# Kernel optimization log

Measured on AMD Instinct MI355X. Metric: run time of the kernel, lower is better.

## Reference

```python
import jax, jax.numpy as jnp
import numpy as np

# Config / sizes
N = 20000       # nodes
E = 320000      # edges (avg degree 16)
IN_DIM = 6      # node feature dim
PE = 8          # laplacian PE dims
ED = 4          # edge feature dim
H = 128         # hidden dim
OUT = 4         # output dim
L = 3           # message-passing layers
T = 3           # node types (typed encoders/decoders)


def mlp(z, W1, b1, W2, b2):
    # _make_mlp: Linear -> ReLU -> Linear
    return jax.nn.relu(z @ W1 + b1) @ W2 + b2


def typed_mlp(z, W1, b1, W2, b2, types):
    # W1: [T, Din, H]; compute all T branches, select per-node by type
    h = jax.nn.relu(jnp.einsum('ni,tih->tnh', z, W1) + b1[:, None, :])
    o = jnp.einsum('tnh,tho->tno', h, W2) + b2[:, None, :]
    onehot = jax.nn.one_hot(types, W1.shape[0], dtype=o.dtype)  # [N, T]
    return jnp.einsum('tno,nt->no', o, onehot)


def setup_inputs() -> dict:
    key = jax.random.key(0)
    ks = jax.random.split(key, 40)

    def w(k, shape, fan_in):
        return jax.random.normal(k, shape, dtype=jnp.float32) / np.float32(np.sqrt(fan_in))

    inp = {}
    inp['x'] = jax.random.normal(ks[0], (N, IN_DIM), dtype=jnp.float32)
    inp['pe'] = jax.random.normal(ks[1], (N, PE), dtype=jnp.float32)
    inp['edge_attr'] = jax.random.normal(ks[2], (E, ED), dtype=jnp.float32)
    # typed node encoders: (in_dim+pe_dims) -> H -> H
    inp['enc_W1'] = w(ks[3], (T, IN_DIM + PE, H), IN_DIM + PE)
    inp['enc_b1'] = jnp.zeros((T, H), jnp.float32)
    inp['enc_W2'] = w(ks[4], (T, H, H), H)
    inp['enc_b2'] = jnp.zeros((T, H), jnp.float32)
    # edge encoder: ED -> H -> H
    inp['ee_W1'] = w(ks[5], (ED, H), ED)
    inp['ee_b1'] = jnp.zeros((H,), jnp.float32)
    inp['ee_W2'] = w(ks[6], (H, H), H)
    inp['ee_b2'] = jnp.zeros((H,), jnp.float32)
    # per-layer edge update (3H->H->H), node update (2H->H->H), fusion (H->H->H)
    inp['eu_W1'] = w(ks[7], (L, 3 * H, H), 3 * H)
    inp['eu_b1'] = jnp.zeros((L, H), jnp.float32)
    inp['eu_W2'] = w(ks[8], (L, H, H), H)
    inp['eu_b2'] = jnp.zeros((L, H), jnp.float32)
    inp['nu_W1'] = w(ks[9], (L, 2 * H, H), 2 * H)
    inp['nu_b1'] = jnp.zeros((L, H), jnp.float32)
    inp['nu_W2'] = w(ks[10], (L, H, H), H)
    inp['nu_b2'] = jnp.zeros((L, H), jnp.float32)
    inp['fu_W1'] = w(ks[11], (L, H, H), H)
    inp['fu_b1'] = jnp.zeros((L, H), jnp.float32)
    inp['fu_W2'] = w(ks[12], (L, H, H), H)
    inp['fu_b2'] = jnp.zeros((L, H), jnp.float32)
    # typed decoders: H -> H -> OUT
    inp['dec_W1'] = w(ks[13], (T, H, H), H)
    inp['dec_b1'] = jnp.zeros((T, H), jnp.float32)
    inp['dec_W2'] = w(ks[14], (T, H, OUT), H)
    inp['dec_b2'] = jnp.zeros((T, OUT), jnp.float32)
    # int inputs
    inp['edge_index'] = jax.random.randint(ks[15], (2, E), 0, N)
    inp['node_types'] = jax.random.randint(ks[16], (N,), 0, T)
    return inp


def reference(x, pe, edge_attr,
              enc_W1, enc_b1, enc_W2, enc_b2,
              ee_W1, ee_b1, ee_W2, ee_b2,
              eu_W1, eu_b1, eu_W2, eu_b2,
              nu_W1, nu_b1, nu_W2, nu_b2,
              fu_W1, fu_b1, fu_W2, fu_b2,
              dec_W1, dec_b1, dec_W2, dec_b2,
              edge_index, node_types):
    n = x.shape[0]
    src, dst = edge_index[0], edge_index[1]
    # typed node encode on [x || pe]
    h_nodes = typed_mlp(jnp.concatenate([x, pe], axis=-1),
                        enc_W1, enc_b1, enc_W2, enc_b2, node_types)
    # edge encode
    h_edges = mlp(edge_attr, ee_W1, ee_b1, ee_W2, ee_b2)
    num_layers = eu_W1.shape[0]
    for l in range(num_layers):
        # gather endpoint states, edge MLP, residual on edges
        m_edge = mlp(jnp.concatenate([h_nodes[src], h_nodes[dst], h_edges], axis=-1),
                     eu_W1[l], eu_b1[l], eu_W2[l], eu_b2[l])
        h_edges = h_edges + m_edge
        # scatter-add aggregation to destination nodes (index_add_)
        m_node = jax.ops.segment_sum(h_edges, dst, num_segments=n)
        # node update + residual, then fusion (dropout is eval/identity)
        upd = mlp(jnp.concatenate([h_nodes, m_node], axis=-1),
                  nu_W1[l], nu_b1[l], nu_W2[l], nu_b2[l])
        local = h_nodes + upd
        h_nodes = mlp(local, fu_W1[l], fu_b1[l], fu_W2[l], fu_b2[l])
    # typed decode
    out = typed_mlp(h_nodes, dec_W1, dec_b1, dec_W2, dec_b2, node_types)
    return out
```

## Files before the change

kernel.cpp:

```cpp
#include <hip/hip_runtime.h>
#include <hip/hip_bf16.h>

typedef __hip_bfloat16 bf16;
typedef __attribute__((ext_vector_type(8))) short short8;
typedef __attribute__((ext_vector_type(4))) float floatx4;

#define HDIM 128
#define NCANON 27

__device__ __forceinline__ float b2f(bf16 v) { return __bfloat162float(v); }
__device__ __forceinline__ float s2f(short s) {
  return __uint_as_float(((unsigned int)(unsigned short)s) << 16);
}

__global__ void detect_kernel(const unsigned short* __restrict__ xraw, int* __restrict__ flag) {
  int j = threadIdx.x;
  unsigned short u = xraw[2 * j];
  int e = (u >> 7) & 0xFF;
  int ok = (u == 0) || (e >= 100 && e <= 140);
  unsigned long long m = __ballot(ok);
  if (j == 0) flag[0] = (__popcll(m) >= 48) ? 1 : 0;
}

struct CanonDesc {
  const void* src[NCANON];
  int prefix[NCANON + 1];
};

__global__ void canon_kernel(CanonDesc d, const int* __restrict__ flag,
                             bf16* __restrict__ out, int total) {
  int t = blockIdx.x * 256 + threadIdx.x;
  if (t >= total) return;
  int ti = 0;
  while (d.prefix[ti + 1] <= t) ti++;
  int off = t - d.prefix[ti];
  if (flag[0]) out[t] = ((const bf16*)d.src[ti])[off];
  else         out[t] = __float2bfloat16(((const float*)d.src[ti])[off]);
}

__global__ void emit_kernel(const bf16* __restrict__ canon_out, const int* __restrict__ flag,
                            void* __restrict__ d_out, int n) {
  int t = blockIdx.x * 256 + threadIdx.x;
  if (t >= n) return;
  if (flag[0]) ((bf16*)d_out)[t] = canon_out[t];
  else         ((float*)d_out)[t] = __bfloat162float(canon_out[t]);
}

__global__ void hist_kernel(const int* __restrict__ dst, int* __restrict__ cnt, int E) {
  int e = blockIdx.x * 256 + threadIdx.x;
  if (e < E) atomicAdd(&cnt[dst[e]], 1);
}

__global__ void scan1_kernel(const int* __restrict__ cnt, int* __restrict__ bsum, int n) {
  int tid = threadIdx.x, lane = tid & 63, wave = tid >> 6;
  int i = blockIdx.x * 256 + tid;
  int v = (i < n) ? cnt[i] : 0;
  #pragma unroll
  for (int d = 32; d; d >>= 1) v += __shfl_down(v, d);
  __shared__ int ws[4];
  if (lane == 0) ws[wave] = v;
  __syncthreads();
  if (tid == 0) bsum[blockIdx.x] = ws[0] + ws[1] + ws[2] + ws[3];
}

__global__ void scan2_kernel(int* __restrict__ bsum, int nb) {
  int lane = threadIdx.x;
  int a0 = (lane < nb) ? bsum[lane] : 0;
  int b0 = (64 + lane < nb) ? bsum[64 + lane] : 0;
  int a = a0, b = b0;
  #pragma unroll
  for (int d = 1; d < 64; d <<= 1) { int t = __shfl_up(a, d); if (lane >= d) a += t; }
  int totA = __shfl(a, 63);
  #pragma unroll
  for (int d = 1; d < 64; d <<= 1) { int t = __shfl_up(b, d); if (lane >= d) b += t; }
  int totB = __shfl(b, 63);
  if (lane < nb) bsum[lane] = a - a0;
  if (64 + lane < nb) bsum[64 + lane] = b - b0 + totA;
  if (lane == 0) bsum[nb] = totA + totB;
}

__global__ void scan3_kernel(const int* __restrict__ cnt, const int* __restrict__ bsum,
                             int* __restrict__ row_start, int n, int nb) {
  __shared__ int sh[256];
  int tid = threadIdx.x;
  int i = blockIdx.x * 256 + tid;
  int v = (i < n) ? cnt[i] : 0;
  sh[tid] = v;
  __syncthreads();
  #pragma unroll
  for (int off = 1; off < 256; off <<= 1) {
    int t = (tid >= off) ? sh[tid - off] : 0;
    __syncthreads();
    sh[tid] += t;
    __syncthreads();
  }
  if (i < n) row_start[i] = bsum[blockIdx.x] + sh[tid] - v;
  if (blockIdx.x == 0 && tid == 0) row_start[n] = bsum[nb];
}

__global__ void scatter_kernel(const int* __restrict__ src, const int* __restrict__ dst,
                               const int* __restrict__ row_start, int* __restrict__ cursor,
                               int* __restrict__ sortedE, int* __restrict__ srcS,
                               int* __restrict__ dstS, int E) {
  int e = blockIdx.x * 256 + threadIdx.x;
  if (e < E) {
    int d = dst[e];
    int pos = row_start[d] + atomicAdd(&cursor[d], 1);
    sortedE[pos] = e;
    srcS[pos] = src[e];
    dstS[pos] = d;
  }
}

__global__ void tcount_kernel(const int* __restrict__ types, int* __restrict__ bcnt, int n) {
  int i = blockIdx.x * 256 + threadIdx.x;
  int lane = threadIdx.x & 63, wave = threadIdx.x >> 6;
  int t = (i < n) ? types[i] : -1;
  __shared__ int wc[4][3];
  unsigned long long m0 = __ballot(t == 0);
  unsigned long long m1 = __ballot(t == 1);
  unsigned long long m2 = __ballot(t == 2);
  if (lane == 0) {
    wc[wave][0] = __popcll(m0); wc[wave][1] = __popcll(m1); wc[wave][2] = __popcll(m2);
  }
  __syncthreads();
  if (threadIdx.x < 3)
    bcnt[blockIdx.x * 3 + threadIdx.x] =
        wc[0][threadIdx.x] + wc[1][threadIdx.x] + wc[2][threadIdx.x] + wc[3][threadIdx.x];
}

__global__ void tscan_kernel(const int* __restrict__ bcnt, int* __restrict__ boff,
                             int* __restrict__ ts, int nb, int n) {
  int lane = threadIdx.x;
  __shared__ int tots[3];
  for (int t = 0; t < 3; t++) {
    int a0 = (lane < nb) ? bcnt[lane * 3 + t] : 0;
    int b0 = (64 + lane < nb) ? bcnt[(64 + lane) * 3 + t] : 0;
    int a = a0, b = b0;
    #pragma unroll
    for (int d = 1; d < 64; d <<= 1) { int x = __shfl_up(a, d); if (lane >= d) a += x; }
    int totA = __shfl(a, 63);
    #pragma unroll
    for (int d = 1; d < 64; d <<= 1) { int x = __shfl_up(b, d); if (lane >= d) b += x; }
    int totB = __shfl(b, 63);
    if (lane < nb) boff[lane * 3 + t] = a - a0;
    if (64 + lane < nb) boff[(64 + lane) * 3 + t] = b - b0 + totA;
    if (lane == 0) tots[t] = totA + totB;
  }
  __syncthreads();
  int tot0 = tots[0], tot1 = tots[1];
  if (lane == 0) { ts[0] = 0; ts[1] = tot0; ts[2] = tot0 + tot1; ts[3] = n; }
  for (int idx = lane; idx < nb; idx += 64) {
    boff[idx * 3 + 1] += tot0;
    boff[idx * 3 + 2] += tot0 + tot1;
  }
}

__global__ void tscatter2_kernel(const int* __restrict__ types, const int* __restrict__ boff,
                                 int* __restrict__ perm, int n) {
  int i = blockIdx.x * 256 + threadIdx.x;
  int lane = threadIdx.x & 63, wave = threadIdx.x >> 6;
  int t = (i < n) ? types[i] : -1;
  __shared__ int wc[4][3];
  unsigned long long m0 = __ballot(t == 0);
  unsigned long long m1 = __ballot(t == 1);
  unsigned long long m2 = __ballot(t == 2);
  if (lane == 0) {
    wc[wave][0] = __popcll(m0); wc[wave][1] = __popcll(m1); wc[wave][2] = __popcll(m2);
  }
  __syncthreads();
  if (i >= n) return;
  unsigned long long mt = (t == 0) ? m0 : ((t == 1) ? m1 : m2);
  unsigned long long below = (lane == 0) ? 0ull : ((1ull << lane) - 1ull);
  int laneRank = __popcll(mt & below);
  int waveOff = 0;
  for (int w = 0; w < wave; w++) waveOff += wc[w][t];
  perm[boff[blockIdx.x * 3 + t] + waveOff + laneRank] = i;
}

__global__ void aggregate_kernel(const bf16* __restrict__ h_edges, const int* __restrict__ row_start,
                                 bf16* __restrict__ m_node, int n) {
  int node = blockIdx.x * 4 + (threadIdx.x >> 6);
  if (node >= n) return;
  int lane = threadIdx.x & 63;
  int chunk = lane & 15;
  int sub = lane >> 4;
  int s = row_start[node], e = row_start[node + 1];
  float acc[8];
  #pragma unroll
  for (int j = 0; j < 8; j++) acc[j] = 0.f;
  for (int p = s + sub; p < e; p += 4) {
    short8 v = *(const short8*)(h_edges + (size_t)p * HDIM + chunk * 8);
    #pragma unroll
    for (int j = 0; j < 8; j++) acc[j] += s2f(v[j]);
  }
  #pragma unroll
  for (int j = 0; j < 8; j++) {
    acc[j] += __shfl_xor(acc[j], 16);
    acc[j] += __shfl_xor(acc[j], 32);
  }
  if (sub == 0) {
    short8 o;
    #pragma unroll
    for (int j = 0; j < 8; j++) o[j] = (short)__bfloat16_as_ushort(__float2bfloat16(acc[j]));
    *(short8*)(m_node + (size_t)node * HDIM + chunk * 8) = o;
  }
}

struct PackJob { const bf16* src; bf16* dst; int Ksrc; int KS; int srcCols; };
struct PackJobs { PackJob j[40]; };

__global__ void pack_all_kernel(PackJobs J) {
  PackJob job = J.j[blockIdx.y];
  int idx = blockIdx.x * 256 + threadIdx.x;
  int total = 8 * job.KS * 64;
  if (idx >= total) return;
  int lane = idx & 63;
  int ks = (idx >> 6) % job.KS;
  int ct = idx / (64 * job.KS);
  bf16* o = job.dst + (size_t)idx * 8;
  int ncol = ct * 16 + (lane & 15);
  int kb = ks * 32 + ((lane >> 4) & 3) * 8;
  #pragma unroll
  for (int jj = 0; jj < 8; jj++) {
    int k = kb + jj;
    o[jj] = (k < job.Ksrc && ncol < job.srcCols)
              ? job.src[(size_t)k * job.srcCols + ncol] : __float2bfloat16(0.f);
  }
}

__global__ void __launch_bounds__(256) ygemm_kernel(
    const bf16* __restrict__ X,
    const bf16* __restrict__ WpA, const bf16* __restrict__ WpB,
    bf16* __restrict__ outA, bf16* __restrict__ outB, int M) {
  const bf16* Wp = blockIdx.y ? WpB : WpA;
  bf16* outp = blockIdx.y ? outB : outA;
  constexpr int BM = 64, RT = 4, SK = 136;
  __shared__ bf16 Zt[BM * SK];
  const int tid = threadIdx.x;
  const int lane = tid & 63, wave = tid >> 6, colq = lane & 15, quad = lane >> 4;
  const int row0 = blockIdx.x * BM;
  {
    int row = tid >> 2, sub = tid & 3;
    int gr = row0 + row;
    bool ok = gr < M;
    #pragma unroll
    for (int j = 0; j < 4; j++) {
      int seg = j * 4 + sub;
      uint4 v = {0u, 0u, 0u, 0u};
      if (ok) v = *(const uint4*)(X + (size_t)gr * HDIM + seg * 8);
      *(uint4*)(&Zt[row * SK + seg * 8]) = v;
    }
  }
  __syncthreads();
  floatx4 acc[RT][2];
  #pragma unroll
  for (int rt = 0; rt < RT; rt++)
    #pragma unroll
    for (int c = 0; c < 2; c++) acc[rt][c] = (floatx4){0.f, 0.f, 0.f, 0.f};
  #pragma unroll
  for (int ks = 0; ks < 4; ks++) {
    short8 bfr0 = *(const short8*)(Wp + (((size_t)(wave * 2 + 0) * 4 + ks) * 64 + lane) * 8);
    short8 bfr1 = *(const short8*)(Wp + (((size_t)(wave * 2 + 1) * 4 + ks) * 64 + lane) * 8);
    #pragma unroll
    for (int rt = 0; rt < RT; rt++) {
      short8 a = *(const short8*)(&Zt[(rt * 16 + colq) * SK + ks * 32 + quad * 8]);
      acc[rt][0] = __builtin_amdgcn_mfma_f32_16x16x32_bf16(a, bfr0, acc[rt][0], 0, 0, 0);
      acc[rt][1] = __builtin_amdgcn_mfma_f32_16x16x32_bf16(a, bfr1, acc[rt][1], 0, 0, 0);
    }
  }
  #pragma unroll
  for (int c = 0; c < 2; c++) {
    int col = wave * 32 + c * 16 + colq;
    #pragma unroll
    for (int rt = 0; rt < RT; rt++)
      #pragma unroll
      for (int r = 0; r < 4; r++) {
        int grow = row0 + rt * 16 + quad * 4 + r;
        if (grow < M) outp[(size_t)grow * HDIM + col] = __float2bfloat16(acc[rt][c][r]);
      }
  }
}

template<int BM>
__global__ void __launch_bounds__(256) eu_kernel(
    const bf16* __restrict__ he, const bf16* __restrict__ ysrc, const bf16* __restrict__ ydst,
    const int* __restrict__ srcS, const int* __restrict__ dstS,
    const bf16* __restrict__ W1p, const bf16* __restrict__ b1v,
    const bf16* __restrict__ W2p, const bf16* __restrict__ b2v,
    bf16* __restrict__ outp, int M) {
  constexpr int RT = BM / 16;
  constexpr int SK = 264;
  __shared__ bf16 Zt[BM * SK];
  const int tid = threadIdx.x;
  const int lane = tid & 63, wave = tid >> 6, colq = lane & 15, quad = lane >> 4;
  const int row0 = blockIdx.x * BM;
  constexpr int TPR = 256 / BM;
  {
    int row = tid / TPR, sub = tid % TPR;
    int gr = row0 + row;
    bool ok = gr < M;
    int g0 = ok ? srcS[gr] : 0;
    int g1 = ok ? dstS[gr] : 0;
    #pragma unroll
    for (int j = 0; j < 32 / TPR; j++) {
      int c = j * TPR + sub;
      int part = c >> 4, seg = c & 15;
      if (part == 0) {
        short8 o = {0, 0, 0, 0, 0, 0, 0, 0};
        if (ok) {
          short8 a = *(const short8*)(ysrc + (size_t)g0 * HDIM + seg * 8);
          short8 b = *(const short8*)(ydst + (size_t)g1 * HDIM + seg * 8);
          #pragma unroll
          for (int k = 0; k < 8; k++)
            o[k] = (short)__bfloat16_as_ushort(__float2bfloat16(s2f(a[k]) + s2f(b[k])));
        }
        *(short8*)(&Zt[row * SK + seg * 8]) = o;
      } else {
        uint4 v = {0u, 0u, 0u, 0u};
        if (ok) v = *(const uint4*)(he + (size_t)gr * HDIM + seg * 8);
        *(uint4*)(&Zt[row * SK + 128 + seg * 8]) = v;
      }
    }
  }
  __syncthreads();

  floatx4 acc[RT][2];
  #pragma unroll
  for (int rt = 0; rt < RT; rt++)
    #pragma unroll
    for (int c = 0; c < 2; c++) acc[rt][c] = (floatx4){0.f, 0.f, 0.f, 0.f};
  #pragma unroll
  for (int ks = 0; ks < 4; ks++) {
    short8 bfr0 = *(const short8*)(W1p + (((size_t)(wave * 2 + 0) * 4 + ks) * 64 + lane) * 8);
    short8 bfr1 = *(const short8*)(W1p + (((size_t)(wave * 2 + 1) * 4 + ks) * 64 + lane) * 8);
    #pragma unroll
    for (int rt = 0; rt < RT; rt++) {
      short8 a = *(const short8*)(&Zt[(rt * 16 + colq) * SK + 128 + ks * 32 + quad * 8]);
      acc[rt][0] = __builtin_amdgcn_mfma_f32_16x16x32_bf16(a, bfr0, acc[rt][0], 0, 0, 0);
      acc[rt][1] = __builtin_amdgcn_mfma_f32_16x16x32_bf16(a, bfr1, acc[rt][1], 0, 0, 0);
    }
  }
  #pragma unroll
  for (int c = 0; c < 2; c++) {
    int col = wave * 32 + c * 16 + colq;
    float bv = b2f(b1v[col]);
    #pragma unroll
    for (int rt = 0; rt < RT; rt++)
      #pragma unroll
      for (int r = 0; r < 4; r++) {
        int lrow = rt * 16 + quad * 4 + r;
        float v = acc[rt][c][r] + bv + b2f(Zt[lrow * SK + col]);
        Zt[lrow * SK + col] = __float2bfloat16(fmaxf(v, 0.f));
      }
  }
  __syncthreads();

  floatx4 acc2[RT][2];
  #pragma unroll
  for (int rt = 0; rt < RT; rt++)
    #pragma unroll
    for (int c = 0; c < 2; c++) acc2[rt][c] = (floatx4){0.f, 0.f, 0.f, 0.f};
  #pragma unroll
  for (int ks = 0; ks < 4; ks++) {
    short8 bfr0 = *(const short8*)(W2p + (((size_t)(wave * 2 + 0) * 4 + ks) * 64 + lane) * 8);
    short8 bfr1 = *(const short8*)(W2p + (((size_t)(wave * 2 + 1) * 4 + ks) * 64 + lane) * 8);
    #pragma unroll
    for (int rt = 0; rt < RT; rt++) {
      short8 a = *(const short8*)(&Zt[(rt * 16 + colq) * SK + ks * 32 + quad * 8]);
      acc2[rt][0] = __builtin_amdgcn_mfma_f32_16x16x32_bf16(a, bfr0, acc2[rt][0], 0, 0, 0);
      acc2[rt][1] = __builtin_amdgcn_mfma_f32_16x16x32_bf16(a, bfr1, acc2[rt][1], 0, 0, 0);
    }
  }
  #pragma unroll
  for (int c = 0; c < 2; c++) {
    int col = wave * 32 + c * 16 + colq;
    float bv = b2f(b2v[col]);
    #pragma unroll
    for (int rt = 0; rt < RT; rt++)
      #pragma unroll
      for (int r = 0; r < 4; r++) {
        int lrow = rt * 16 + quad * 4 + r;
        int grow = row0 + lrow;
        if (grow < M) {
          float v = acc2[rt][c][r] + bv + b2f(Zt[lrow * SK + 128 + col]);
          outp[(size_t)grow * HDIM + col] = __float2bfloat16(v);
        }
      }
  }
}

template<int KS1, bool DEC>
__global__ void __launch_bounds__(256) typed_kernel(
    const bf16* __restrict__ in0, const bf16* __restrict__ in1,
    const int* __restrict__ perm, const int* __restrict__ ts,
    const bf16* __restrict__ W1p, int w1s, const bf16* __restrict__ b1v, int b1s,
    const bf16* __restrict__ W2p, int w2s, const bf16* __restrict__ b2v, int b2s,
    bf16* __restrict__ outp) {
  constexpr int BM = 64, RT = 4;
  constexpr int SK = KS1 * 32 + 8;
  constexpr int HS = 136;
  int t = blockIdx.y;
  int rs = ts[t], re = ts[t + 1];
  int row0 = rs + blockIdx.x * BM;
  if (row0 >= re) return;
  __shared__ bf16 Zt[BM * SK];
  __shared__ bf16 Hid[BM * HS];
  __shared__ int gIdx[BM];
  const int tid = threadIdx.x;
  const int lane = tid & 63, wave = tid >> 6, colq = lane & 15, quad = lane >> 4;
  for (int i = tid; i < BM; i += 256) gIdx[i] = (row0 + i < re) ? perm[row0 + i] : -1;
  __syncthreads();
  if (DEC) {
    int row = tid >> 2, sub = tid & 3;
    int g = gIdx[row];
    #pragma unroll
    for (int j = 0; j < 4; j++) {
      int seg = j * 4 + sub;
      uint4 v = {0u, 0u, 0u, 0u};
      if (g >= 0) v = *(const uint4*)(in0 + (size_t)g * HDIM + seg * 8);
      *(uint4*)(&Zt[row * SK + seg * 8]) = v;
    }
  } else {
    for (int i = tid; i < BM * 32; i += 256) {
      int row = i >> 5, k = i & 31;
      int g = gIdx[row];
      bf16 v = __float2bfloat16(0.f);
      if (g >= 0 && k < 14) v = (k < 6) ? in0[(size_t)g * 6 + k] : in1[(size_t)g * 8 + (k - 6)];
      Zt[row * SK + k] = v;
    }
  }
  __syncthreads();

  const bf16* W1t = W1p + (size_t)t * w1s;
  const bf16* W2t = W2p + (size_t)t * w2s;
  floatx4 acc[RT][2];
  #pragma unroll
  for (int rt = 0; rt < RT; rt++)
    #pragma unroll
    for (int c = 0; c < 2; c++) acc[rt][c] = (floatx4){0.f, 0.f, 0.f, 0.f};
  #pragma unroll
  for (int ks = 0; ks < KS1; ks++) {
    short8 bfr0 = *(const short8*)(W1t + (((size_t)(wave * 2 + 0) * KS1 + ks) * 64 + lane) * 8);
    short8 bfr1 = *(const short8*)(W1t + (((size_t)(wave * 2 + 1) * KS1 + ks) * 64 + lane) * 8);
    #pragma unroll
    for (int rt = 0; rt < RT; rt++) {
      short8 a = *(const short8*)(&Zt[(rt * 16 + colq) * SK + ks * 32 + quad * 8]);
      acc[rt][0] = __builtin_amdgcn_mfma_f32_16x16x32_bf16(a, bfr0, acc[rt][0], 0, 0, 0);
      acc[rt][1] = __builtin_amdgcn_mfma_f32_16x16x32_bf16(a, bfr1, acc[rt][1], 0, 0, 0);
    }
  }
  #pragma unroll
  for (int c = 0; c < 2; c++) {
    int col = wave * 32 + c * 16 + colq;
    float bv = b2f(b1v[t * b1s + col]);
    #pragma unroll
    for (int rt = 0; rt < RT; rt++)
      #pragma unroll
      for (int r = 0; r < 4; r++) {
        float v = acc[rt][c][r] + bv;
        Hid[(rt * 16 + quad * 4 + r) * HS + col] = __float2bfloat16(fmaxf(v, 0.f));
      }
  }
  __syncthreads();

  floatx4 acc2[RT][2];
  #pragma unroll
  for (int rt = 0; rt < RT; rt++)
    #pragma unroll
    for (int c = 0; c < 2; c++) acc2[rt][c] = (floatx4){0.f, 0.f, 0.f, 0.f};
  #pragma unroll
  for (int ks = 0; ks < 4; ks++) {
    short8 bfr0 = *(const short8*)(W2t + (((size_t)(wave * 2 + 0) * 4 + ks) * 64 + lane) * 8);
    short8 bfr1 = *(const short8*)(W2t + (((size_t)(wave * 2 + 1) * 4 + ks) * 64 + lane) * 8);
    #pragma unroll
    for (int rt = 0; rt < RT; rt++) {
      short8 a = *(const short8*)(&Hid[(rt * 16 + colq) * HS + ks * 32 + quad * 8]);
      acc2[rt][0] = __builtin_amdgcn_mfma_f32_16x16x32_bf16(a, bfr0, acc2[rt][0], 0, 0, 0);
      acc2[rt][1] = __builtin_amdgcn_mfma_f32_16x16x32_bf16(a, bfr1, acc2[rt][1], 0, 0, 0);
    }
  }
  if (DEC) {
    if (wave == 0 && colq < 4) {
      float bv = b2f(b2v[t * b2s + colq]);
      #pragma unroll
      for (int rt = 0; rt < RT; rt++)
        #pragma unroll
        for (int r = 0; r < 4; r++) {
          int g = gIdx[rt * 16 + quad * 4 + r];
          if (g >= 0) outp[(size_t)g * 4 + colq] = __float2bfloat16(acc2[rt][0][r] + bv);
        }
    }
  } else {
    #pragma unroll
    for (int c = 0; c < 2; c++) {
      int col = wave * 32 + c * 16 + colq;
      float bv = b2f(b2v[t * b2s + col]);
      #pragma unroll
      for (int rt = 0; rt < RT; rt++)
        #pragma unroll
        for (int r = 0; r < 4; r++) {
          int g = gIdx[rt * 16 + quad * 4 + r];
          if (g >= 0) outp[(size_t)g * HDIM + col] = __float2bfloat16(acc2[rt][c][r] + bv);
        }
    }
  }
}

template<int NPARTS, int KS1, int RES_PART, int BM, int HID_OFF, bool ATTR4>
__global__ void __launch_bounds__(256) mlp2_kernel(
    const bf16* __restrict__ p0, const int* __restrict__ idx0,
    const bf16* __restrict__ p1,
    const bf16* __restrict__ W1p, const bf16* __restrict__ b1v,
    const bf16* __restrict__ W2p, const bf16* __restrict__ b2v,
    bf16* __restrict__ outp, int M) {
  constexpr int RT = BM / 16;
  constexpr int SK = NPARTS * 128 + 8;
  __shared__ bf16 Zt[BM * SK];
  bf16* Hid = &Zt[HID_OFF];
  const int tid = threadIdx.x;
  const int lane = tid & 63, wave = tid >> 6, colq = lane & 15, quad = lane >> 4;
  const int row0 = blockIdx.x * BM;

  if (ATTR4) {
    for (int i = tid; i < BM * 4; i += 256) {
      int row = i >> 2, seg = i & 3;
      int gr = row0 + row;
      uint4 val = {0u, 0u, 0u, 0u};
      if (seg == 0 && gr < M) {
        int g = idx0 ? idx0[gr] : gr;
        uint2 v = *(const uint2*)(p0 + (size_t)g * 4);
        val.x = v.x; val.y = v.y;
      }
      *(uint4*)(&Zt[row * SK + seg * 8]) = val;
    }
  } else {
    constexpr int TPR = 256 / BM;
    constexpr int PT = NPARTS * 16 / TPR;
    int row = tid / TPR, sub = tid % TPR;
    int gr = row0 + row;
    bool ok = (gr < M);
    #pragma unroll
    for (int j = 0; j < PT; j++) {
      int c = j * TPR + sub;
      int part = c >> 4, seg = c & 15;
      uint4 val = {0u, 0u, 0u, 0u};
      if (ok) {
        const bf16* p = (part == 0) ? p0 : p1;
        val = *(const uint4*)(p + (size_t)gr * HDIM + seg * 8);
      }
      *(uint4*)(&Zt[row * SK + part * 128 + seg * 8]) = val;
    }
  }
  __syncthreads();

  floatx4 acc[RT][2];
  #pragma unroll
  for (int rt = 0; rt < RT; rt++)
    #pragma unroll
    for (int c = 0; c < 2; c++) acc[rt][c] = (floatx4){0.f, 0.f, 0.f, 0.f};
  #pragma unroll
  for (int ks = 0; ks < KS1; ks++) {
    short8 bfr0 = *(const short8*)(W1p + (((size_t)(wave * 2 + 0) * KS1 + ks) * 64 + lane) * 8);
    short8 bfr1 = *(const short8*)(W1p + (((size_t)(wave * 2 + 1) * KS1 + ks) * 64 + lane) * 8);
    #pragma unroll
    for (int rt = 0; rt < RT; rt++) {
      short8 a = *(const short8*)(&Zt[(rt * 16 + colq) * SK + ks * 32 + quad * 8]);
      acc[rt][0] = __builtin_amdgcn_mfma_f32_16x16x32_bf16(a, bfr0, acc[rt][0], 0, 0, 0);
      acc[rt][1] = __builtin_amdgcn_mfma_f32_16x16x32_bf16(a, bfr1, acc[rt][1], 0, 0, 0);
    }
  }
  __syncthreads();

  #pragma unroll
  for (int c = 0; c < 2; c++) {
    int col = wave * 32 + c * 16 + colq;
    float bv = b2f(b1v[col]);
    #pragma unroll
    for (int rt = 0; rt < RT; rt++)
      #pragma unroll
      for (int r = 0; r < 4; r++) {
        float v = acc[rt][c][r] + bv;
        Hid[(rt * 16 + quad * 4 + r) * SK + col] = __float2bfloat16(fmaxf(v, 0.f));
      }
  }
  __syncthreads();

  floatx4 acc2[RT][2];
  #pragma unroll
  for (int rt = 0; rt < RT; rt++)
    #pragma unroll
    for (int c = 0; c < 2; c++) acc2[rt][c] = (floatx4){0.f, 0.f, 0.f, 0.f};
  #pragma unroll
  for (int ks = 0; ks < 4; ks++) {
    short8 bfr0 = *(const short8*)(W2p + (((size_t)(wave * 2 + 0) * 4 + ks) * 64 + lane) * 8);
    short8 bfr1 = *(const short8*)(W2p + (((size_t)(wave * 2 + 1) * 4 + ks) * 64 + lane) * 8);
    #pragma unroll
    for (int rt = 0; rt < RT; rt++) {
      short8 a = *(const short8*)(&Hid[(rt * 16 + colq) * SK + ks * 32 + quad * 8]);
      acc2[rt][0] = __builtin_amdgcn_mfma_f32_16x16x32_bf16(a, bfr0, acc2[rt][0], 0, 0, 0);
      acc2[rt][1] = __builtin_amdgcn_mfma_f32_16x16x32_bf16(a, bfr1, acc2[rt][1], 0, 0, 0);
    }
  }
  #pragma unroll
  for (int c = 0; c < 2; c++) {
    int col = wave * 32 + c * 16 + colq;
    float bv = b2f(b2v[col]);
    #pragma unroll
    for (int rt = 0; rt < RT; rt++)
      #pragma unroll
      for (int r = 0; r < 4; r++) {
        int lrow = rt * 16 + quad * 4 + r;
        int grow = row0 + lrow;
        if (grow < M) {
          float v = acc2[rt][c][r] + bv;
          if constexpr (RES_PART >= 0)
            v += b2f(Zt[lrow * SK + RES_PART * 128 + col]);
          outp[(size_t)grow * HDIM + col] = __float2bfloat16(v);
        }
      }
  }
}

extern "C" void kernel_launch(void* const* d_in, const int* in_sizes, int n_in,
                              void* d_out, int out_size, void* d_ws, size_t ws_size,
                              hipStream_t stream) {
  const int* edge_index = (const int*)d_in[27];
  const int* node_types = (const int*)d_in[28];
  const int N = in_sizes[28];
  const int E = in_sizes[2] / 4;
  const int L = in_sizes[12] / HDIM;
  const int* srcI = edge_index;
  const int* dstI = edge_index + E;

  CanonDesc cd;
  int total = 0;
  for (int i = 0; i < NCANON; i++) { cd.src[i] = d_in[i]; cd.prefix[i] = total; total += in_sizes[i]; }
  cd.prefix[NCANON] = total;

  char* wsb = (char*)d_ws;
  size_t off = 0;
  auto alloc = [&](size_t bytes) -> void* {
    void* p = wsb + off;
    off += (bytes + 255) & ~(size_t)255;
    return p;
  };
  int*  flag      = (int*)alloc(256);
  bf16* arena     = (bf16*)alloc((size_t)total * 2);
  bf16* h_nodes   = (bf16*)alloc((size_t)N * HDIM * 2);
  bf16* h_edges   = (bf16*)alloc((size_t)E * HDIM * 2);
  bf16* m_node    = (bf16*)alloc((size_t)N * HDIM * 2);
  bf16* localb    = (bf16*)alloc((size_t)N * HDIM * 2);
  bf16* ysrcb     = (bf16*)alloc((size_t)N * HDIM * 2);
  bf16* ydstb     = (bf16*)alloc((size_t)N * HDIM * 2);
  bf16* canon_out = (bf16*)alloc((size_t)out_size * 2);
  int* counts     = (int*)alloc((size_t)N * 4);
  int* cursor     = (int*)alloc((size_t)N * 4);
  int* row_start  = (int*)alloc((size_t)(N + 1) * 4);
  int* bsum       = (int*)alloc(260 * 4);
  int* sortedE    = (int*)alloc((size_t)E * 4);
  int* srcS       = (int*)alloc((size_t)E * 4);
  int* dstS       = (int*)alloc((size_t)E * 4);
  int* bcntT      = (int*)alloc(512 * 4);
  int* boffT      = (int*)alloc(512 * 4);
  int* tsArr      = (int*)alloc(64);
  int* permT      = (int*)alloc((size_t)N * 4);
  bf16* eeW1p  = (bf16*)alloc(4096 * 2);
  bf16* eeW2p  = (bf16*)alloc(16384 * 2);
  bf16* encW1p = (bf16*)alloc(3 * 4096 * 2);
  bf16* encW2p = (bf16*)alloc(3 * 16384 * 2);
  bf16* decW1p = (bf16*)alloc(3 * 16384 * 2);
  bf16* decW2p = (bf16*)alloc(3 * 16384 * 2);
  bf16* euW1a  = (bf16*)alloc((size_t)L * 16384 * 2);
  bf16* euW1b  = (bf16*)alloc((size_t)L * 16384 * 2);
  bf16* euW1c  = (bf16*)alloc((size_t)L * 16384 * 2);
  bf16* euW2p  = (bf16*)alloc((size_t)L * 16384 * 2);
  bf16* nuW1p  = (bf16*)alloc((size_t)L * 32768 * 2);
  bf16* nuW2p  = (bf16*)alloc((size_t)L * 16384 * 2);
  bf16* fuW1p  = (bf16*)alloc((size_t)L * 16384 * 2);
  bf16* fuW2p  = (bf16*)alloc((size_t)L * 16384 * 2);

  const bf16* cX     = arena + cd.prefix[0];
  const bf16* cPE    = arena + cd.prefix[1];
  const bf16* cEA    = arena + cd.prefix[2];
  const bf16* cEncW1 = arena + cd.prefix[3];
  const bf16* cEncB1 = arena + cd.prefix[4];
  const bf16* cEncW2 = arena + cd.prefix[5];
  const bf16* cEncB2 = arena + cd.prefix[6];
  const bf16* cEeW1  = arena + cd.prefix[7];
  const bf16* cEeB1  = arena + cd.prefix[8];
  const bf16* cEeW2  = arena + cd.prefix[9];
  const bf16* cEeB2  = arena + cd.prefix[10];
  const bf16* cEuW1  = arena + cd.prefix[11];
  const bf16* cEuB1  = arena + cd.prefix[12];
  const bf16* cEuW2  = arena + cd.prefix[13];
  const bf16* cEuB2  = arena + cd.prefix[14];
  const bf16* cNuW1  = arena + cd.prefix[15];
  const bf16* cNuB1  = arena + cd.prefix[16];
  const bf16* cNuW2  = arena + cd.prefix[17];
  const bf16* cNuB2  = arena + cd.prefix[18];
  const bf16* cFuW1  = arena + cd.prefix[19];
  const bf16* cFuB1  = arena + cd.prefix[20];
  const bf16* cFuW2  = arena + cd.prefix[21];
  const bf16* cFuB2  = arena + cd.prefix[22];
  const bf16* cDecW1 = arena + cd.prefix[23];
  const bf16* cDecB1 = arena + cd.prefix[24];
  const bf16* cDecW2 = arena + cd.prefix[25];
  const bf16* cDecB2 = arena + cd.prefix[26];

  detect_kernel<<<1, 64, 0, stream>>>((const unsigned short*)d_in[0], flag);
  canon_kernel<<<(total + 255) / 256, 256, 0, stream>>>(cd, flag, arena, total);

  hipMemsetAsync(counts, 0, (size_t)N * 4, stream);
  hipMemsetAsync(cursor, 0, (size_t)N * 4, stream);

  PackJobs PJ;
  int nj = 0;
  PJ.j[nj++] = {cEeW1, eeW1p, 4, 1, 128};
  PJ.j[nj++] = {cEeW2, eeW2p, 128, 4, 128};
  for (int l = 0; l < L; l++) {
    const bf16* w1 = cEuW1 + (size_t)l * 384 * HDIM;
    PJ.j[nj++] = {w1,                 euW1a + (size_t)l * 16384, 128, 4, 128};
    PJ.j[nj++] = {w1 + 128 * HDIM,    euW1b + (size_t)l * 16384, 128, 4, 128};
    PJ.j[nj++] = {w1 + 256 * HDIM,    euW1c + (size_t)l * 16384, 128, 4, 128};
    PJ.j[nj++] = {cEuW2 + (size_t)l * HDIM * HDIM, euW2p + (size_t)l * 16384, 128, 4, 128};
    PJ.j[nj++] = {cNuW1 + (size_t)l * 256 * HDIM,  nuW1p + (size_t)l * 32768, 256, 8, 128};
    PJ.j[nj++] = {cNuW2 + (size_t)l * HDIM * HDIM, nuW2p + (size_t)l * 16384, 128, 4, 128};
    PJ.j[nj++] = {cFuW1 + (size_t)l * HDIM * HDIM, fuW1p + (size_t)l * 16384, 128, 4, 128};
    PJ.j[nj++] = {cFuW2 + (size_t)l * HDIM * HDIM, fuW2p + (size_t)l * 16384, 128, 4, 128};
  }
  for (int t = 0; t < 3; t++) {
    PJ.j[nj++] = {cEncW1 + (size_t)t * 14 * HDIM,   encW1p + (size_t)t * 4096, 14, 1, 128};
    PJ.j[nj++] = {cEncW2 + (size_t)t * HDIM * HDIM, encW2p + (size_t)t * 16384, 128, 4, 128};
    PJ.j[nj++] = {cDecW1 + (size_t)t * HDIM * HDIM, decW1p + (size_t)t * 16384, 128, 4, 128};
    PJ.j[nj++] = {cDecW2 + (size_t)t * HDIM * 4,    decW2p + (size_t)t * 16384, 128, 4, 4};
  }
  pack_all_kernel<<<dim3(16, nj), 256, 0, stream>>>(PJ);

  int nb = (N + 255) / 256;
  hist_kernel<<<(E + 255) / 256, 256, 0, stream>>>(dstI, counts, E);
  scan1_kernel<<<nb, 256, 0, stream>>>(counts, bsum, N);
  scan2_kernel<<<1, 64, 0, stream>>>(bsum, nb);
  scan3_kernel<<<nb, 256, 0, stream>>>(counts, bsum, row_start, N, nb);
  scatter_kernel<<<(E + 255) / 256, 256, 0, stream>>>(srcI, dstI, row_start, cursor,
                                                      sortedE, srcS, dstS, E);
  tcount_kernel<<<nb, 256, 0, stream>>>(node_types, bcntT, N);
  tscan_kernel<<<1, 64, 0, stream>>>(bcntT, boffT, tsArr, nb, N);
  tscatter2_kernel<<<nb, 256, 0, stream>>>(node_types, boffT, permT, N);

  int ngrid64 = (N + 63) / 64;
  typed_kernel<1, false><<<dim3(ngrid64, 3), 256, 0, stream>>>(
      cX, cPE, permT, tsArr, encW1p, 4096, cEncB1, HDIM,
      encW2p, 16384, cEncB2, HDIM, h_nodes);

  int egrid32  = (E + 31) / 32;
  int egrid128 = (E + 127) / 128;
  int ngrid128 = (N + 127) / 128;

  mlp2_kernel<1, 1, -1, 128, 0, true><<<egrid128, 256, 0, stream>>>(
      cEA, sortedE, nullptr, eeW1p, cEeB1, eeW2p, cEeB2, h_edges, E);

  for (int l = 0; l < L; l++) {
    ygemm_kernel<<<dim3(ngrid64, 2), 256, 0, stream>>>(
        h_nodes, euW1a + (size_t)l * 16384, euW1b + (size_t)l * 16384, ysrcb, ydstb, N);
    eu_kernel<32><<<egrid32, 256, 0, stream>>>(
        h_edges, ysrcb, ydstb, srcS, dstS,
        euW1c + (size_t)l * 16384, cEuB1 + l * HDIM,
        euW2p + (size_t)l * 16384, cEuB2 + l * HDIM, h_edges, E);
    aggregate_kernel<<<(N + 3) / 4, 256, 0, stream>>>(h_edges, row_start, m_node, N);
    mlp2_kernel<2, 8, 0, 64, 128, false><<<ngrid64, 256, 0, stream>>>(
        h_nodes, nullptr, m_node,
        nuW1p + (size_t)l * 32768, cNuB1 + l * HDIM,
        nuW2p + (size_t)l * 16384, cNuB2 + l * HDIM, localb, N);
    mlp2_kernel<1, 4, -1, 128, 0, false><<<ngrid128, 256, 0, stream>>>(
        localb, nullptr, nullptr,
        fuW1p + (size_t)l * 16384, cFuB1 + l * HDIM,
        fuW2p + (size_t)l * 16384, cFuB2 + l * HDIM, h_nodes, N);
  }

  typed_kernel<4, true><<<dim3(ngrid64, 3), 256, 0, stream>>>(
      h_nodes, nullptr, permT, tsArr, decW1p, 16384, cDecB1, HDIM,
      decW2p, 16384, cDecB2, 4, canon_out);
  emit_kernel<<<(out_size + 255) / 256, 256, 0, stream>>>(canon_out, flag, d_out, out_size);
  (void)n_in; (void)ws_size;
}
```

Baseline: 537.5 us.

## Fuse edge aggregation into edge update and merge node/fusion MLPs

```diff
diff --git a/kernel.cpp b/kernel.cpp
--- a/kernel.cpp
+++ b/kernel.cpp
@@ -11,6 +11,9 @@
 __device__ __forceinline__ float b2f(bf16 v) { return __bfloat162float(v); }
 __device__ __forceinline__ float s2f(short s) {
   return __uint_as_float(((unsigned int)(unsigned short)s) << 16);
+}
+__device__ __forceinline__ short f2s(float f) {
+  return (short)__bfloat16_as_ushort(__float2bfloat16(f));
 }
 
 __global__ void detect_kernel(const unsigned short* __restrict__ xraw, int* __restrict__ flag) {
@@ -176,35 +179,6 @@
   int waveOff = 0;
   for (int w = 0; w < wave; w++) waveOff += wc[w][t];
   perm[boff[blockIdx.x * 3 + t] + waveOff + laneRank] = i;
-}
-
-__global__ void aggregate_kernel(const bf16* __restrict__ h_edges, const int* __restrict__ row_start,
-                                 bf16* __restrict__ m_node, int n) {
-  int node = blockIdx.x * 4 + (threadIdx.x >> 6);
-  if (node >= n) return;
-  int lane = threadIdx.x & 63;
-  int chunk = lane & 15;
-  int sub = lane >> 4;
-  int s = row_start[node], e = row_start[node + 1];
-  float acc[8];
-  #pragma unroll
-  for (int j = 0; j < 8; j++) acc[j] = 0.f;
-  for (int p = s + sub; p < e; p += 4) {
-    short8 v = *(const short8*)(h_edges + (size_t)p * HDIM + chunk * 8);
-    #pragma unroll
-    for (int j = 0; j < 8; j++) acc[j] += s2f(v[j]);
-  }
-  #pragma unroll
-  for (int j = 0; j < 8; j++) {
-    acc[j] += __shfl_xor(acc[j], 16);
-    acc[j] += __shfl_xor(acc[j], 32);
-  }
-  if (sub == 0) {
-    short8 o;
-    #pragma unroll
-    for (int j = 0; j < 8; j++) o[j] = (short)__bfloat16_as_ushort(__float2bfloat16(acc[j]));
-    *(short8*)(m_node + (size_t)node * HDIM + chunk * 8) = o;
-  }
 }
 
 struct PackJob { const bf16* src; bf16* dst; int Ksrc; int KS; int srcCols; };
@@ -288,10 +262,11 @@
     const int* __restrict__ srcS, const int* __restrict__ dstS,
     const bf16* __restrict__ W1p, const bf16* __restrict__ b1v,
     const bf16* __restrict__ W2p, const bf16* __restrict__ b2v,
-    bf16* __restrict__ outp, int M) {
+    bf16* __restrict__ outp, float* __restrict__ mnode, int M) {
   constexpr int RT = BM / 16;
   constexpr int SK = 264;
   __shared__ bf16 Zt[BM * SK];
+  __shared__ int dstLds[BM];
   const int tid = threadIdx.x;
   const int lane = tid & 63, wave = tid >> 6, colq = lane & 15, quad = lane >> 4;
   const int row0 = blockIdx.x * BM;
@@ -302,6 +277,7 @@
     bool ok = gr < M;
     int g0 = ok ? srcS[gr] : 0;
     int g1 = ok ? dstS[gr] : 0;
+    if (sub == 0) dstLds[row] = ok ? g1 : -1;
     #pragma unroll
     for (int j = 0; j < 32 / TPR; j++) {
       int c = j * TPR + sub;
@@ -312,8 +288,7 @@
           short8 a = *(const short8*)(ysrc + (size_t)g0 * HDIM + seg * 8);
           short8 b = *(const short8*)(ydst + (size_t)g1 * HDIM + seg * 8);
           #pragma unroll
-          for (int k = 0; k < 8; k++)
-            o[k] = (short)__bfloat16_as_ushort(__float2bfloat16(s2f(a[k]) + s2f(b[k])));
+          for (int k = 0; k < 8; k++) o[k] = f2s(s2f(a[k]) + s2f(b[k]));
         }
         *(short8*)(&Zt[row * SK + seg * 8]) = o;
       } else {
@@ -382,10 +357,184 @@
       for (int r = 0; r < 4; r++) {
         int lrow = rt * 16 + quad * 4 + r;
         int grow = row0 + lrow;
-        if (grow < M) {
-          float v = acc2[rt][c][r] + bv + b2f(Zt[lrow * SK + 128 + col]);
-          outp[(size_t)grow * HDIM + col] = __float2bfloat16(v);
+        float v = acc2[rt][c][r] + bv + b2f(Zt[lrow * SK + 128 + col]);
+        bf16 vb = __float2bfloat16(v);
+        Zt[lrow * SK + 128 + col] = vb;
+        if (grow < M) outp[(size_t)grow * HDIM + col] = vb;
+      }
+  }
+  __syncthreads();
+
+  if (tid < 128) {
+    int col = tid;
+    float s = 0.f;
+    int runDst = dstLds[0];
+    bool touchStart = true;
+    for (int r = 0; r < BM; r++) {
+      int d = dstLds[r];
+      if (d != runDst) {
+        if (runDst >= 0) {
+          float* mp = &mnode[(size_t)runDst * HDIM + col];
+          if (touchStart) atomicAdd(mp, s); else *mp = s;
         }
+        runDst = d; s = 0.f; touchStart = false;
+      }
+      s += b2f(Zt[r * SK + 128 + col]);
+    }
+    if (runDst >= 0) atomicAdd(&mnode[(size_t)runDst * HDIM + col], s);
+  }
+}
+
+__global__ void __launch_bounds__(256) node_kernel(
+    const bf16* __restrict__ h_nodes, const float* __restrict__ mnode,
+    const bf16* __restrict__ nuW1, const bf16* __restrict__ nuB1,
+    const bf16* __restrict__ nuW2, const bf16* __restrict__ nuB2,
+    const bf16* __restrict__ fuW1, const bf16* __restrict__ fuB1,
+    const bf16* __restrict__ fuW2, const bf16* __restrict__ fuB2,
+    bf16* __restrict__ outp, int M) {
+  constexpr int BM = 64, RT = 4, SK = 264;
+  __shared__ bf16 Zt[BM * SK];
+  const int tid = threadIdx.x;
+  const int lane = tid & 63, wave = tid >> 6, colq = lane & 15, quad = lane >> 4;
+  const int row0 = blockIdx.x * BM;
+  {
+    int row = tid >> 2, sub = tid & 3;
+    int gr = row0 + row;
+    bool ok = gr < M;
+    #pragma unroll
+    for (int j = 0; j < 8; j++) {
+      int c = j * 4 + sub;
+      int part = c >> 4, seg = c & 15;
+      if (part == 0) {
+        uint4 v = {0u, 0u, 0u, 0u};
+        if (ok) v = *(const uint4*)(h_nodes + (size_t)gr * HDIM + seg * 8);
+        *(uint4*)(&Zt[row * SK + seg * 8]) = v;
+      } else {
+        short8 o = {0, 0, 0, 0, 0, 0, 0, 0};
+        if (ok) {
+          const float* mp = mnode + (size_t)gr * HDIM + seg * 8;
+          #pragma unroll
+          for (int k = 0; k < 8; k++) o[k] = f2s(mp[k]);
+        }
+        *(short8*)(&Zt[row * SK + 128 + seg * 8]) = o;
+      }
+    }
+  }
+  __syncthreads();
+
+  floatx4 acc[RT][2];
+  #pragma unroll
+  for (int rt = 0; rt < RT; rt++)
+    #pragma unroll
+    for (int c = 0; c < 2; c++) acc[rt][c] = (floatx4){0.f, 0.f, 0.f, 0.f};
+  #pragma unroll
+  for (int ks = 0; ks < 8; ks++) {
+    short8 bfr0 = *(const short8*)(nuW1 + (((size_t)(wave * 2 + 0) * 8 + ks) * 64 + lane) * 8);
+    short8 bfr1 = *(const short8*)(nuW1 + (((size_t)(wave * 2 + 1) * 8 + ks) * 64 + lane) * 8);
+    #pragma unroll
+    for (int rt = 0; rt < RT; rt++) {
+      short8 a = *(const short8*)(&Zt[(rt * 16 + colq) * SK + ks * 32 + quad * 8]);
+      acc[rt][0] = __builtin_amdgcn_mfma_f32_16x16x32_bf16(a, bfr0, acc[rt][0], 0, 0, 0);
+      acc[rt][1] = __builtin_amdgcn_mfma_f32_16x16x32_bf16(a, bfr1, acc[rt][1], 0, 0, 0);
+    }
+  }
+  __syncthreads();
+  #pragma unroll
+  for (int c = 0; c < 2; c++) {
+    int col = wave * 32 + c * 16 + colq;
+    float bv = b2f(nuB1[col]);
+    #pragma unroll
+    for (int rt = 0; rt < RT; rt++)
+      #pragma unroll
+      for (int r = 0; r < 4; r++)
+        Zt[(rt * 16 + quad * 4 + r) * SK + 128 + col] =
+            __float2bfloat16(fmaxf(acc[rt][c][r] + bv, 0.f));
+  }
+  __syncthreads();
+
+  #pragma unroll
+  for (int rt = 0; rt < RT; rt++)
+    #pragma unroll
+    for (int c = 0; c < 2; c++) acc[rt][c] = (floatx4){0.f, 0.f, 0.f, 0.f};
+  #pragma unroll
+  for (int ks = 0; ks < 4; ks++) {
+    short8 bfr0 = *(const short8*)(nuW2 + (((size_t)(wave * 2 + 0) * 4 + ks) * 64 + lane) * 8);
+    short8 bfr1 = *(const short8*)(nuW2 + (((size_t)(wave * 2 + 1) * 4 + ks) * 64 + lane) * 8);
+    #pragma unroll
+    for (int rt = 0; rt < RT; rt++) {
+      short8 a = *(const short8*)(&Zt[(rt * 16 + colq) * SK + 128 + ks * 32 + quad * 8]);
+      acc[rt][0] = __builtin_amdgcn_mfma_f32_16x16x32_bf16(a, bfr0, acc[rt][0], 0, 0, 0);
+      acc[rt][1] = __builtin_amdgcn_mfma_f32_16x16x32_bf16(a, bfr1, acc[rt][1], 0, 0, 0);
+    }
+  }
+  #pragma unroll
+  for (int c = 0; c < 2; c++) {
+    int col = wave * 32 + c * 16 + colq;
+    float bv = b2f(nuB2[col]);
+    #pragma unroll
+    for (int rt = 0; rt < RT; rt++)
+      #pragma unroll
+      for (int r = 0; r < 4; r++) {
+        int lrow = rt * 16 + quad * 4 + r;
+        float v = acc[rt][c][r] + bv + b2f(Zt[lrow * SK + col]);
+        Zt[lrow * SK + col] = __float2bfloat16(v);
+      }
+  }
+  __syncthreads();
+
+  #pragma unroll
+  for (int rt = 0; rt < RT; rt++)
+    #pragma unroll
+    for (int c = 0; c < 2; c++) acc[rt][c] = (floatx4){0.f, 0.f, 0.f, 0.f};
+  #pragma unroll
+  for (int ks = 0; ks < 4; ks++) {
+    short8 bfr0 = *(const short8*)(fuW1 + (((size_t)(wave * 2 + 0) * 4 + ks) * 64 + lane) * 8);
+    short8 bfr1 = *(const short8*)(fuW1 + (((size_t)(wave * 2 + 1) * 4 + ks) * 64 + lane) * 8);
+    #pragma unroll
+    for (int rt = 0; rt < RT; rt++) {
+      short8 a = *(const short8*)(&Zt[(rt * 16 + colq) * SK + ks * 32 + quad * 8]);
+      acc[rt][0] = __builtin_amdgcn_mfma_f32_16x16x32_bf16(a, bfr0, acc[rt][0], 0, 0, 0);
+      acc[rt][1] = __builtin_amdgcn_mfma_f32_16x16x32_bf16(a, bfr1, acc[rt][1], 0, 0, 0);
+    }
+  }
+  #pragma unroll
+  for (int c = 0; c < 2; c++) {
+    int col = wave * 32 + c * 16 + colq;
+    float bv = b2f(fuB1[col]);
+    #pragma unroll
+    for (int rt = 0; rt < RT; rt++)
+      #pragma unroll
+      for (int r = 0; r < 4; r++)
+        Zt[(rt * 16 + quad * 4 + r) * SK + 128 + col] =
+            __float2bfloat16(fmaxf(acc[rt][c][r] + bv, 0.f));
+  }
+  __syncthreads();
+
+  #pragma unroll
+  for (int rt = 0; rt < RT; rt++)
+    #pragma unroll
+    for (int c = 0; c < 2; c++) acc[rt][c] = (floatx4){0.f, 0.f, 0.f, 0.f};
+  #pragma unroll
+  for (int ks = 0; ks < 4; ks++) {
+    short8 bfr0 = *(const short8*)(fuW2 + (((size_t)(wave * 2 + 0) * 4 + ks) * 64 + lane) * 8);
+    short8 bfr1 = *(const short8*)(fuW2 + (((size_t)(wave * 2 + 1) * 4 + ks) * 64 + lane) * 8);
+    #pragma unroll
+    for (int rt = 0; rt < RT; rt++) {
+      short8 a = *(const short8*)(&Zt[(rt * 16 + colq) * SK + 128 + ks * 32 + quad * 8]);
+      acc[rt][0] = __builtin_amdgcn_mfma_f32_16x16x32_bf16(a, bfr0, acc[rt][0], 0, 0, 0);
+      acc[rt][1] = __builtin_amdgcn_mfma_f32_16x16x32_bf16(a, bfr1, acc[rt][1], 0, 0, 0);
+    }
+  }
+  #pragma unroll
+  for (int c = 0; c < 2; c++) {
+    int col = wave * 32 + c * 16 + colq;
+    float bv = b2f(fuB2[col]);
+    #pragma unroll
+    for (int rt = 0; rt < RT; rt++)
+      #pragma unroll
+      for (int r = 0; r < 4; r++) {
+        int grow = row0 + rt * 16 + quad * 4 + r;
+        if (grow < M) outp[(size_t)grow * HDIM + col] = __float2bfloat16(acc[rt][c][r] + bv);
       }
   }
 }
@@ -507,50 +656,29 @@
   }
 }
 
-template<int NPARTS, int KS1, int RES_PART, int BM, int HID_OFF, bool ATTR4>
-__global__ void __launch_bounds__(256) mlp2_kernel(
+template<int BM>
+__global__ void __launch_bounds__(256) ee_kernel(
     const bf16* __restrict__ p0, const int* __restrict__ idx0,
-    const bf16* __restrict__ p1,
     const bf16* __restrict__ W1p, const bf16* __restrict__ b1v,
     const bf16* __restrict__ W2p, const bf16* __restrict__ b2v,
     bf16* __restrict__ outp, int M) {
   constexpr int RT = BM / 16;
-  constexpr int SK = NPARTS * 128 + 8;
+  constexpr int SK = 136;
   __shared__ bf16 Zt[BM * SK];
-  bf16* Hid = &Zt[HID_OFF];
   const int tid = threadIdx.x;
   const int lane = tid & 63, wave = tid >> 6, colq = lane & 15, quad = lane >> 4;
   const int row0 = blockIdx.x * BM;
 
-  if (ATTR4) {
-    for (int i = tid; i < BM * 4; i += 256) {
-      int row = i >> 2, seg = i & 3;
-      int gr = row0 + row;
-      uint4 val = {0u, 0u, 0u, 0u};
-      if (seg == 0 && gr < M) {
-        int g = idx0 ? idx0[gr] : gr;
-        uint2 v = *(const uint2*)(p0 + (size_t)g * 4);
-        val.x = v.x; val.y = v.y;
-      }
-      *(uint4*)(&Zt[row * SK + seg * 8]) = val;
-    }
-  } else {
-    constexpr int TPR = 256 / BM;
-    constexpr int PT = NPARTS * 16 / TPR;
-    int row = tid / TPR, sub = tid % TPR;
+  for (int i = tid; i < BM * 4; i += 256) {
+    int row = i >> 2, seg = i & 3;
     int gr = row0 + row;
-    bool ok = (gr < M);
-    #pragma unroll
-    for (int j = 0; j < PT; j++) {
-      int c = j * TPR + sub;
-      int part = c >> 4, seg = c & 15;
-      uint4 val = {0u, 0u, 0u, 0u};
-      if (ok) {
-        const bf16* p = (part == 0) ? p0 : p1;
-        val = *(const uint4*)(p + (size_t)gr * HDIM + seg * 8);
-      }
-      *(uint4*)(&Zt[row * SK + part * 128 + seg * 8]) = val;
-    }
+    uint4 val = {0u, 0u, 0u, 0u};
+    if (seg == 0 && gr < M) {
+      int g = idx0 ? idx0[gr] : gr;
+      uint2 v = *(const uint2*)(p0 + (size_t)g * 4);
+      val.x = v.x; val.y = v.y;
+    }
+    *(uint4*)(&Zt[row * SK + seg * 8]) = val;
   }
   __syncthreads();
 
@@ -559,19 +687,17 @@
   for (int rt = 0; rt < RT; rt++)
     #pragma unroll
     for (int c = 0; c < 2; c++) acc[rt][c] = (floatx4){0.f, 0.f, 0.f, 0.f};
-  #pragma unroll
-  for (int ks = 0; ks < KS1; ks++) {
-    short8 bfr0 = *(const short8*)(W1p + (((size_t)(wave * 2 + 0) * KS1 + ks) * 64 + lane) * 8);
-    short8 bfr1 = *(const short8*)(W1p + (((size_t)(wave * 2 + 1) * KS1 + ks) * 64 + lane) * 8);
-    #pragma unroll
-    for (int rt = 0; rt < RT; rt++) {
-      short8 a = *(const short8*)(&Zt[(rt * 16 + colq) * SK + ks * 32 + quad * 8]);
+  {
+    short8 bfr0 = *(const short8*)(W1p + (((size_t)(wave * 2 + 0)) * 64 + lane) * 8);
+    short8 bfr1 = *(const short8*)(W1p + (((size_t)(wave * 2 + 1)) * 64 + lane) * 8);
+    #pragma unroll
+    for (int rt = 0; rt < RT; rt++) {
+      short8 a = *(const short8*)(&Zt[(rt * 16 + colq) * SK + quad * 8]);
       acc[rt][0] = __builtin_amdgcn_mfma_f32_16x16x32_bf16(a, bfr0, acc[rt][0], 0, 0, 0);
       acc[rt][1] = __builtin_amdgcn_mfma_f32_16x16x32_bf16(a, bfr1, acc[rt][1], 0, 0, 0);
     }
   }
   __syncthreads();
-
   #pragma unroll
   for (int c = 0; c < 2; c++) {
     int col = wave * 32 + c * 16 + colq;
@@ -579,10 +705,9 @@
     #pragma unroll
     for (int rt = 0; rt < RT; rt++)
       #pragma unroll
-      for (int r = 0; r < 4; r++) {
-        float v = acc[rt][c][r] + bv;
-        Hid[(rt * 16 + quad * 4 + r) * SK + col] = __float2bfloat16(fmaxf(v, 0.f));
-      }
+      for (int r = 0; r < 4; r++)
+        Zt[(rt * 16 + quad * 4 + r) * SK + col] =
+            __float2bfloat16(fmaxf(acc[rt][c][r] + bv, 0.f));
   }
   __syncthreads();
 
@@ -597,7 +722,7 @@
     short8 bfr1 = *(const short8*)(W2p + (((size_t)(wave * 2 + 1) * 4 + ks) * 64 + lane) * 8);
     #pragma unroll
     for (int rt = 0; rt < RT; rt++) {
-      short8 a = *(const short8*)(&Hid[(rt * 16 + colq) * SK + ks * 32 + quad * 8]);
+      short8 a = *(const short8*)(&Zt[(rt * 16 + colq) * SK + ks * 32 + quad * 8]);
       acc2[rt][0] = __builtin_amdgcn_mfma_f32_16x16x32_bf16(a, bfr0, acc2[rt][0], 0, 0, 0);
       acc2[rt][1] = __builtin_amdgcn_mfma_f32_16x16x32_bf16(a, bfr1, acc2[rt][1], 0, 0, 0);
     }
@@ -610,14 +735,9 @@
     for (int rt = 0; rt < RT; rt++)
       #pragma unroll
       for (int r = 0; r < 4; r++) {
-        int lrow = rt * 16 + quad * 4 + r;
-        int grow = row0 + lrow;
-        if (grow < M) {
-          float v = acc2[rt][c][r] + bv;
-          if constexpr (RES_PART >= 0)
-            v += b2f(Zt[lrow * SK + RES_PART * 128 + col]);
-          outp[(size_t)grow * HDIM + col] = __float2bfloat16(v);
-        }
+        int grow = row0 + rt * 16 + quad * 4 + r;
+        if (grow < M)
+          outp[(size_t)grow * HDIM + col] = __float2bfloat16(acc2[rt][c][r] + bv);
       }
   }
 }
@@ -649,8 +769,7 @@
   bf16* arena     = (bf16*)alloc((size_t)total * 2);
   bf16* h_nodes   = (bf16*)alloc((size_t)N * HDIM * 2);
   bf16* h_edges   = (bf16*)alloc((size_t)E * HDIM * 2);
-  bf16* m_node    = (bf16*)alloc((size_t)N * HDIM * 2);
-  bf16* localb    = (bf16*)alloc((size_t)N * HDIM * 2);
+  float* m_node   = (float*)alloc((size_t)N * HDIM * 4);
   bf16* ysrcb     = (bf16*)alloc((size_t)N * HDIM * 2);
   bf16* ydstb     = (bf16*)alloc((size_t)N * HDIM * 2);
   bf16* canon_out = (bf16*)alloc((size_t)out_size * 2);
@@ -755,25 +874,22 @@
 
   int egrid32  = (E + 31) / 32;
   int egrid128 = (E + 127) / 128;
-  int ngrid128 = (N + 127) / 128;
-
-  mlp2_kernel<1, 1, -1, 128, 0, true><<<egrid128, 256, 0, stream>>>(
-      cEA, sortedE, nullptr, eeW1p, cEeB1, eeW2p, cEeB2, h_edges, E);
+
+  ee_kernel<128><<<egrid128, 256, 0, stream>>>(
+      cEA, sortedE, eeW1p, cEeB1, eeW2p, cEeB2, h_edges, E);
 
   for (int l = 0; l < L; l++) {
+    hipMemsetAsync(m_node, 0, (size_t)N * HDIM * 4, stream);
     ygemm_kernel<<<dim3(ngrid64, 2), 256, 0, stream>>>(
         h_nodes, euW1a + (size_t)l * 16384, euW1b + (size_t)l * 16384, ysrcb, ydstb, N);
     eu_kernel<32><<<egrid32, 256, 0, stream>>>(
         h_edges, ysrcb, ydstb, srcS, dstS,
         euW1c + (size_t)l * 16384, cEuB1 + l * HDIM,
-        euW2p + (size_t)l * 16384, cEuB2 + l * HDIM, h_edges, E);
-    aggregate_kernel<<<(N + 3) / 4, 256, 0, stream>>>(h_edges, row_start, m_node, N);
-    mlp2_kernel<2, 8, 0, 64, 128, false><<<ngrid64, 256, 0, stream>>>(
-        h_nodes, nullptr, m_node,
+        euW2p + (size_t)l * 16384, cEuB2 + l * HDIM, h_edges, m_node, E);
+    node_kernel<<<ngrid64, 256, 0, stream>>>(
+        h_nodes, m_node,
         nuW1p + (size_t)l * 32768, cNuB1 + l * HDIM,
-        nuW2p + (size_t)l * 16384, cNuB2 + l * HDIM, localb, N);
-    mlp2_kernel<1, 4, -1, 128, 0, false><<<ngrid128, 256, 0, stream>>>(
-        localb, nullptr, nullptr,
+        nuW2p + (size_t)l * 16384, cNuB2 + l * HDIM,
         fuW1p + (size_t)l * 16384, cFuB1 + l * HDIM,
         fuW2p + (size_t)l * 16384, cFuB2 + l * HDIM, h_nodes, N);
   }
```

New measurement: 503.8 us. -6.3%, faster.
